# Kernel tuning notes

Measured on AMD Instinct MI355X. Metric: run time of the kernel, lower is better.

## Reference

```python
import jax, jax.numpy as jnp
import numpy as np
from jax import lax

B, C, K, H, W = 32, 256, 64, 64, 64  # batch, num_channels, num_corr_channels, spatial
IN = C + K  # enc input channels = 320
EPS = 1e-5


def setup_inputs() -> dict:
    key = jax.random.key(0)
    ks = jax.random.split(key, 20)
    n = lambda k, s, sc=0.05: jax.random.normal(k, s, dtype=jnp.float32) * sc
    return {
        "z": jax.random.normal(ks[0], (B, C, K), dtype=jnp.float32),
        "x": jax.random.normal(ks[1], (B, C, H, W), dtype=jnp.float32),
        "d": jax.random.normal(ks[2], (B, C, H, W), dtype=jnp.float32),
        # ConvBlock: depthwise [IN,1,3,3] + pointwise [C,IN]
        "dw_w": n(ks[3], (IN, 1, 3, 3), 0.1),
        "dw_b": n(ks[4], (IN,)),
        "pw_w": n(ks[5], (C, IN), 0.05),
        "pw_b": n(ks[6], (C,)),
        # BatchNorm2d (inference-mode running stats)
        "bn_gamma": 1.0 + n(ks[7], (C,)),
        "bn_beta": n(ks[8], (C,)),
        "bn_mean": n(ks[9], (C,)),
        "bn_var": 0.5 + jax.random.uniform(ks[10], (C,), dtype=jnp.float32),
        # SelfAttention: 1x1 conv projections + q/k/v linears
        "inp_w": n(ks[11], (C, C)), "inp_b": n(ks[12], (C,)),
        "q_w": n(ks[13], (C, C)), "q_b": n(ks[14], (C,)),
        "k_w": n(ks[15], (C, C)), "k_b": n(ks[16], (C,)),
        "v_w": n(ks[17], (C, C)), "v_b": n(ks[18], (C,)),
        "op_w": n(ks[19], (C, C)), "op_b": jnp.zeros((C,), jnp.float32),
    }


def reference(z, x, d, dw_w, dw_b, pw_w, pw_b, bn_gamma, bn_beta, bn_mean, bn_var,
              inp_w, inp_b, q_w, q_b, k_w, k_b, v_w, v_b, op_w, op_b):
    b, c, h, w = x.shape
    # correlation: z^T @ x_flat -> [b, K, h*w] -> [b, K, h, w]
    s = jnp.einsum('bck,bcn->bkn', z, x.reshape(b, c, h * w)).reshape(b, -1, h, w)
    s = jnp.concatenate([s, d], axis=1)  # [b, C+K, h, w]
    # depthwise 3x3 (pad 1) + pointwise 1x1
    s = lax.conv_general_dilated(s, dw_w, (1, 1), [(1, 1), (1, 1)],
                                 dimension_numbers=('NCHW', 'OIHW', 'NCHW'),
                                 feature_group_count=s.shape[1]) + dw_b[:, None, None]
    s = jnp.einsum('bihw,oi->bohw', s, pw_w) + pw_b[:, None, None]
    # BN (inference) + ReLU
    s = (s - bn_mean[:, None, None]) * lax.rsqrt(bn_var[:, None, None] + EPS)
    s = jnp.maximum(s * bn_gamma[:, None, None] + bn_beta[:, None, None], 0.0)
    # channel self-attention
    px = jnp.einsum('bchw,oc->bohw', s, inp_w) + inp_b[:, None, None]
    flat = px.reshape(b, c, h * w).transpose(0, 2, 1)  # [b, n, c]
    q = flat @ q_w.T + q_b
    k = flat @ k_w.T + k_b
    v = flat @ v_w.T + v_b
    score = jnp.einsum('bnc,bnd->bcd', q, k) / (c ** 0.5)  # [b, c, c]
    att = jax.nn.softmax(score, axis=2)
    weighted = jnp.einsum('bnc,bcd->bnd', v, att)  # values @ attention
    wt = weighted.transpose(0, 2, 1).reshape(b, c, h, w)
    out = jnp.einsum('bchw,oc->bohw', wt, op_w) + op_b[:, None, None]
    return out + s
```

## Files before the change

kernel.cpp:

```cpp
#include <hip/hip_runtime.h>

static constexpr int B_ = 32, C_ = 256, K_ = 64, H_ = 64, W_ = 64;
static constexpr int N_ = H_ * W_;
static constexpr int IN_ = C_ + K_;

__device__ __forceinline__ short f2bs(float f) {
  unsigned u = __builtin_bit_cast(unsigned, f);
  u += 0x7fffu + ((u >> 16) & 1u);
  return (short)(u >> 16);
}
__device__ __forceinline__ float bs2f(short s) {
  unsigned u = ((unsigned)(unsigned short)s) << 16;
  return __builtin_bit_cast(float, u);
}

typedef __attribute__((ext_vector_type(8))) short s8v;
typedef __attribute__((ext_vector_type(4))) short s4v;
typedef __attribute__((ext_vector_type(4))) float f4v;

static constexpr long long OB_XT   = 0;
static constexpr long long OB_ZT   = 67108864LL;
static constexpr long long OB_DWS  = 0;
static constexpr long long OB_DT   = 83886080LL;
static constexpr long long OB_PX   = 83886080LL;
static constexpr long long OB_CORR = 150994944LL;
static constexpr long long OB_G    = 150994944LL;
static constexpr long long OB_GB2  = 159383552LL;
static constexpr long long OB_S    = 167772160LL;
static constexpr long long OB_PXT  = 234881024LL;
static constexpr long long OB_ATT  = 301989888LL;
static constexpr long long OB_M2   = OB_ATT + 8388608LL;
static constexpr long long OB_M3   = OB_M2 + 8388608LL;
static constexpr long long OB_MISC = OB_M3 + 8388608LL;
static constexpr long long OB_PWW  = OB_MISC;
static constexpr long long OB_INPW = OB_PWW + 262144LL;
static constexpr long long OB_M3B  = OB_INPW + 262144LL;
static constexpr long long OB_R    = OB_M3B + 4194304LL;
static constexpr long long OB_U    = OB_R + 32768LL;
static constexpr long long OB_W2   = OB_U + 32768LL;
static constexpr long long OB_M2B  = OB_W2 + 32768LL;
static constexpr long long OB_B3   = OB_M2B + 32768LL;
static constexpr long long OB_BNS  = OB_B3 + 32768LL;
static constexpr long long OB_BNH  = OB_BNS + 2048LL;
static constexpr long long OB_QW2  = OB_BNH + 2048LL;
static constexpr long long OB_KWB  = OB_QW2 + 262144LL;
static constexpr long long OB_VWB  = OB_KWB + 131072LL;
static constexpr long long OB_OPWB = OB_VWB + 131072LL;
static constexpr long long OB_T1B  = OB_OPWB + 131072LL;
static constexpr long long OB_ATTT = OB_T1B + 4194304LL;
static constexpr long long OB_M2T  = OB_ATTT + 4194304LL;
static constexpr long long OB_VWT  = OB_M2T + 4194304LL;

__device__ __forceinline__ void gload16(const void* g, void* l) {
  __builtin_amdgcn_global_load_lds((const __attribute__((address_space(1))) void*)g,
                                   (__attribute__((address_space(3))) void*)l, 16, 0, 0);
}

template <int BN, int SPLIT, int EPI>
__global__ __launch_bounds__(256) void mgemm(
    const short* __restrict__ A, int lda, long long sA,
    const short* __restrict__ Bt, int ldb, long long sB,
    void* __restrict__ Cv, int ldc, long long sC,
    int Kd,
    const float* __restrict__ biasc, const float* __restrict__ shf,
    const float* __restrict__ biasr,
    const short* __restrict__ resT, int ldrt, long long sRT,
    short* __restrict__ outT, int ldt, long long sT)
{
  constexpr int JT = BN / 32;
  __shared__ short As[128 * 32];
  __shared__ short Bs[BN * 32];

  const int t = threadIdx.x;
  const int wv = t >> 6;
  const int lane = t & 63, quad = lane >> 4, lr = lane & 15;
  const int wm = wv >> 1, wn = wv & 1;
  const int m_off = wm * 64, n_off = wn * (BN / 2);

  const int n0 = blockIdx.x * BN;
  const int m0 = blockIdx.y * 128;
  const int bz = (SPLIT == 1) ? blockIdx.z : (blockIdx.z / SPLIT);
  const int sp = (SPLIT == 1) ? 0 : (blockIdx.z % SPLIT);
  const int koff = sp * Kd;

  A += (long long)bz * sA;
  Bt += (long long)bz * sB;

  const int arow = t >> 2;
  const int acol = (t & 3) << 3;

  f4v acc[4][JT];
#pragma unroll
  for (int i = 0; i < 4; ++i)
#pragma unroll
    for (int j = 0; j < JT; ++j) acc[i][j] = (f4v)0.f;

  for (int k0 = 0; k0 < Kd; k0 += 32) {
#pragma unroll
    for (int rr = 0; rr < 2; ++rr) {
      const short* gp = A + (long long)(m0 + rr * 64 + arow) * lda + koff + k0 + acol;
      gload16(gp, (char*)As + rr * 4096 + wv * 1024);
    }
#pragma unroll
    for (int rr = 0; rr < BN / 64; ++rr) {
      const short* gp = Bt + (long long)(n0 + rr * 64 + arow) * ldb + koff + k0 + acol;
      gload16(gp, (char*)Bs + rr * 4096 + wv * 1024);
    }
    __syncthreads();

    s8v af[4], bfv[JT];
#pragma unroll
    for (int i = 0; i < 4; ++i)
      af[i] = *(const s8v*)&As[(m_off + i * 16 + lr) * 32 + quad * 8];
#pragma unroll
    for (int j = 0; j < JT; ++j)
      bfv[j] = *(const s8v*)&Bs[(n_off + j * 16 + lr) * 32 + quad * 8];
#pragma unroll
    for (int i = 0; i < 4; ++i)
#pragma unroll
      for (int j = 0; j < JT; ++j)
        acc[i][j] = __builtin_amdgcn_mfma_f32_16x16x32_bf16(af[i], bfv[j], acc[i][j], 0, 0, 0);
    __syncthreads();
  }

  float* Cf = (float*)Cv;
  short* Cb = (short*)Cv;
  if (EPI & 1) Cb += (long long)bz * sC; else Cf += (long long)bz * sC;
  if (EPI & 16) resT += (long long)bz * sRT;
  if (EPI & 32) outT += (long long)bz * sT;

#pragma unroll
  for (int i = 0; i < 4; ++i) {
    const int mb = m0 + m_off + i * 16 + quad * 4;
#pragma unroll
    for (int j = 0; j < JT; ++j) {
      const int n = n0 + n_off + j * 16 + lr;
      float vr[4];
#pragma unroll
      for (int r = 0; r < 4; ++r) {
        float v = acc[i][j][r];
        if (EPI & 2) v += biasc[n];
        if (EPI & 4) v = fmaxf(fmaf(v, biasc[n], shf[n]), 0.f);
        if (EPI & 8) v += biasr[bz * 256 + mb + r];
        vr[r] = v;
      }
      if (EPI & 16) {
        s4v rv = *(const s4v*)(resT + (long long)n * ldrt + mb);
#pragma unroll
        for (int r = 0; r < 4; ++r) vr[r] += bs2f(rv[r]);
      }
      if (EPI & 32) {
        s4v tv;
#pragma unroll
        for (int r = 0; r < 4; ++r) tv[r] = f2bs(vr[r]);
        *(s4v*)(outT + (long long)n * ldt + mb) = tv;
      }
#pragma unroll
      for (int r = 0; r < 4; ++r) {
        if (EPI & 64) atomicAdd(&Cf[(long long)(mb + r) * ldc + n], vr[r]);
        else if (EPI & 1) Cb[(long long)(mb + r) * ldc + n] = f2bs(vr[r]);
        else Cf[(long long)(mb + r) * ldc + n] = vr[r];
      }
    }
  }
}

__global__ __launch_bounds__(256) void tcast(const float* __restrict__ in,
                                             short* __restrict__ out,
                                             int R, int Cc, long long sIn, long long sOut)
{
  __shared__ float tile[32][33];
  const int b = blockIdx.z;
  const int r0 = blockIdx.y * 32, c0 = blockIdx.x * 32;
  in += (long long)b * sIn;
  out += (long long)b * sOut;
  const int tx = threadIdx.x & 31, ty = threadIdx.x >> 5;
#pragma unroll
  for (int i = 0; i < 32; i += 8)
    tile[ty + i][tx] = in[(long long)(r0 + ty + i) * Cc + c0 + tx];
  __syncthreads();
#pragma unroll
  for (int i = 0; i < 32; i += 8)
    out[(long long)(c0 + ty + i) * R + r0 + tx] = f2bs(tile[tx][ty + i]);
}

__global__ void castw(const float* __restrict__ in, short* __restrict__ out, long long n)
{
  long long i = (long long)blockIdx.x * 256 + threadIdx.x;
  if (i < n) out[i] = f2bs(in[i]);
}

__global__ void castw2(const float* __restrict__ a, const float* __restrict__ b,
                       short* __restrict__ oa, short* __restrict__ ob)
{
  const int i = blockIdx.x * 256 + threadIdx.x;
  const int sel = i >> 16, off = i & 65535;
  const float* src = sel == 0 ? a : b;
  short* dst = sel == 0 ? oa : ob;
  dst[off] = f2bs(src[off]);
}

__global__ void qdup(const float* __restrict__ q, short* __restrict__ o)
{
  const int i = blockIdx.x * 256 + threadIdx.x;
  const short v = f2bs(q[i]);
  const int c = i >> 8, e = i & 255;
  o[c * 512 + e] = v;
  o[c * 512 + 256 + e] = v;
}

__global__ void ghilo(const float* __restrict__ G, short* __restrict__ g2)
{
  const long long i = (long long)blockIdx.x * 256 + threadIdx.x;
  const float g = G[i];
  const short h = f2bs(g);
  const short l = f2bs(g - bs2f(h));
  const long long row = i >> 8;
  const int e = (int)(i & 255);
  g2[row * 512 + e] = h;
  g2[row * 512 + 256 + e] = l;
}

__global__ __launch_bounds__(256) void dwconv4(const short* __restrict__ corr,
                                               const short* __restrict__ dt,
                                               const float* __restrict__ wgt,
                                               const float* __restrict__ bias,
                                               short* __restrict__ outp)
{
  __shared__ __align__(16) float wl[9 * IN_];
  __shared__ __align__(16) float bl[IN_];
  const int tid = threadIdx.x;
  for (int i = tid; i < 9 * IN_; i += 256) {
    const int ch = i / 9, tap = i % 9;
    wl[tap * IN_ + ch] = wgt[i];
  }
  for (int i = tid; i < IN_; i += 256) bl[i] = bias[i];
  __syncthreads();

  const int g = blockIdx.x * 256 + tid;
  const int b = blockIdx.y;
  const int cg = g % 40;
  const int rest = g / 40;
  const int x = rest & 63;
  const int y0 = (rest >> 6) << 2;
  const int ch0 = cg * 8;

  const short* base;
  int ldch, c0;
  if (cg < 8) { base = corr + (long long)b * N_ * K_; ldch = K_; c0 = ch0; }
  else        { base = dt   + (long long)b * N_ * C_; ldch = C_; c0 = ch0 - K_; }

  float acc[4][8];
  {
    float4 bv0 = *(const float4*)&bl[ch0];
    float4 bv1 = *(const float4*)&bl[ch0 + 4];
#pragma unroll
    for (int p = 0; p < 4; ++p) {
      acc[p][0] = bv0.x; acc[p][1] = bv0.y; acc[p][2] = bv0.z; acc[p][3] = bv0.w;
      acc[p][4] = bv1.x; acc[p][5] = bv1.y; acc[p][6] = bv1.z; acc[p][7] = bv1.w;
    }
  }

#pragma unroll
  for (int dx = -1; dx <= 1; ++dx) {
    const int xx = x + dx;
    if (xx < 0 || xx >= W_) continue;

    float wv[3][8];
#pragma unroll
    for (int dy1 = 0; dy1 < 3; ++dy1) {
      float4 wa = *(const float4*)&wl[(dy1 * 3 + (dx + 1)) * IN_ + ch0];
      float4 wb = *(const float4*)&wl[(dy1 * 3 + (dx + 1)) * IN_ + ch0 + 4];
      wv[dy1][0] = wa.x; wv[dy1][1] = wa.y; wv[dy1][2] = wa.z; wv[dy1][3] = wa.w;
      wv[dy1][4] = wb.x; wv[dy1][5] = wb.y; wv[dy1][6] = wb.z; wv[dy1][7] = wb.w;
    }

    s8v v[6];
#pragma unroll
    for (int ri = 0; ri < 6; ++ri) {
      const int yy = y0 - 1 + ri;
      if (yy >= 0 && yy < H_)
        v[ri] = *(const s8v*)(base + (long long)(yy * W_ + xx) * ldch + c0);
      else
        v[ri] = (s8v)0;
    }

#pragma unroll
    for (int ri = 0; ri < 6; ++ri) {
      float f[8];
#pragma unroll
      for (int j = 0; j < 8; ++j) f[j] = bs2f(v[ri][j]);
#pragma unroll
      for (int dy1 = 0; dy1 < 3; ++dy1) {
        const int p = ri - dy1;
        if (p < 0 || p > 3) continue;
#pragma unroll
        for (int j = 0; j < 8; ++j)
          acc[p][j] = fmaf(wv[dy1][j], f[j], acc[p][j]);
      }
    }
  }

#pragma unroll
  for (int p = 0; p < 4; ++p) {
    s8v o;
#pragma unroll
    for (int j = 0; j < 8; ++j) o[j] = f2bs(acc[p][j]);
    *(s8v*)(outp + ((long long)b * N_ + (y0 + p) * W_ + x) * IN_ + ch0) = o;
  }
}

__global__ void colsum(const short* __restrict__ px, float* __restrict__ r)
{
  const int b = blockIdx.y, c = threadIdx.x, chunk = blockIdx.x;
  const short* p = px + (long long)b * N_ * C_ + (long long)chunk * 512 * C_;
  float s = 0.f;
  for (int n = 0; n < 512; ++n) s += bs2f(p[(long long)n * C_ + c]);
  atomicAdd(&r[b * C_ + c], s);
}

__global__ void bncoef(const float* __restrict__ pwb, const float* __restrict__ g,
                       const float* __restrict__ bt, const float* __restrict__ mn,
                       const float* __restrict__ vr, float* __restrict__ scl,
                       float* __restrict__ shf)
{
  const int c = threadIdx.x;
  const float inv = rsqrtf(vr[c] + 1e-5f);
  const float sc = g[c] * inv;
  scl[c] = sc;
  shf[c] = (pwb[c] - mn[c]) * sc + bt[c];
}

__global__ void uwker(const float* __restrict__ qw, const float* __restrict__ kw,
                      const float* __restrict__ r, float* __restrict__ u,
                      float* __restrict__ w)
{
  const int b = blockIdx.x, c = threadIdx.x;
  __shared__ float rl[256];
  rl[c] = r[b * C_ + c];
  __syncthreads();
  float su = 0.f, sw = 0.f;
  for (int f = 0; f < C_; ++f) {
    const float rv = rl[f];
    su = fmaf(qw[c * C_ + f], rv, su);
    sw = fmaf(kw[c * C_ + f], rv, sw);
  }
  u[b * C_ + c] = su;
  w[b * C_ + c] = sw;
}

__global__ void fixsoftmax(float* __restrict__ att, const float* __restrict__ u,
                           const float* __restrict__ w, const float* __restrict__ qb,
                           const float* __restrict__ kb)
{
  const int c = blockIdx.x, b = blockIdx.y, d = threadIdx.x;
  const long long base = ((long long)b * C_ + c) * (long long)C_;
  const float qbc = qb[c];
  float val = 0.0625f * (att[base + d] + u[b * C_ + c] * kb[d] + qbc * w[b * C_ + d] +
                         (float)N_ * qbc * kb[d]);
  __shared__ float red[256];
  red[d] = val;
  __syncthreads();
  for (int k = 128; k > 0; k >>= 1) {
    if (d < k) red[d] = fmaxf(red[d], red[d + k]);
    __syncthreads();
  }
  const float mx = red[0];
  __syncthreads();
  const float e = expf(val - mx);
  red[d] = e;
  __syncthreads();
  for (int k = 128; k > 0; k >>= 1) {
    if (d < k) red[d] += red[d + k];
    __syncthreads();
  }
  att[base + d] = e / red[0];
}

__global__ void m2bker(const float* __restrict__ att, const float* __restrict__ vb,
                       float* __restrict__ m2b)
{
  const int b = blockIdx.x, d = threadIdx.x;
  const float* a = att + (long long)b * C_ * C_;
  float s = 0.f;
  for (int c = 0; c < C_; ++c) s = fmaf(a[c * C_ + d], vb[c], s);
  m2b[b * C_ + d] = s;
}

__global__ void b3ker(const float* __restrict__ opw, const float* __restrict__ m2b,
                      const float* __restrict__ opb, float* __restrict__ b3)
{
  const int b = blockIdx.x, o = threadIdx.x;
  __shared__ float m[256];
  m[o] = m2b[b * C_ + o];
  __syncthreads();
  float s = opb[o];
  for (int d = 0; d < C_; ++d) s = fmaf(opw[o * C_ + d], m[d], s);
  b3[b * C_ + o] = s;
}

extern "C" void kernel_launch(void* const* d_in, const int* in_sizes, int n_in,
                              void* d_out, int out_size, void* d_ws, size_t ws_size,
                              hipStream_t stream)
{
  (void)in_sizes; (void)n_in; (void)out_size; (void)ws_size;
  const float* z     = (const float*)d_in[0];
  const float* x     = (const float*)d_in[1];
  const float* dimg  = (const float*)d_in[2];
  const float* dw_w  = (const float*)d_in[3];
  const float* dw_b  = (const float*)d_in[4];
  const float* pw_w  = (const float*)d_in[5];
  const float* pw_b  = (const float*)d_in[6];
  const float* bn_g  = (const float*)d_in[7];
  const float* bn_b  = (const float*)d_in[8];
  const float* bn_m  = (const float*)d_in[9];
  const float* bn_v  = (const float*)d_in[10];
  const float* inp_w = (const float*)d_in[11];
  const float* inp_b = (const float*)d_in[12];
  const float* q_w   = (const float*)d_in[13];
  const float* q_b   = (const float*)d_in[14];
  const float* k_w   = (const float*)d_in[15];
  const float* k_b   = (const float*)d_in[16];
  const float* v_w   = (const float*)d_in[17];
  const float* v_b   = (const float*)d_in[18];
  const float* op_w  = (const float*)d_in[19];
  const float* op_b  = (const float*)d_in[20];
  float* out = (float*)d_out;

  char* ws = (char*)d_ws;
  short* xt    = (short*)(ws + OB_XT);
  short* zt    = (short*)(ws + OB_ZT);
  short* dws   = (short*)(ws + OB_DWS);
  short* dt    = (short*)(ws + OB_DT);
  short* px_b  = (short*)(ws + OB_PX);
  short* corr  = (short*)(ws + OB_CORR);
  float* G     = (float*)(ws + OB_G);
  short* Gb2   = (short*)(ws + OB_GB2);
  short* s_b   = (short*)(ws + OB_S);
  short* pxT   = (short*)(ws + OB_PXT);
  float* att   = (float*)(ws + OB_ATT);
  short* M2scr = (short*)(ws + OB_M2);
  short* pw_wb = (short*)(ws + OB_PWW);
  short* inp_wb= (short*)(ws + OB_INPW);
  short* M3b   = (short*)(ws + OB_M3B);
  float* r     = (float*)(ws + OB_R);
  float* u     = (float*)(ws + OB_U);
  float* w2    = (float*)(ws + OB_W2);
  float* m2b   = (float*)(ws + OB_M2B);
  float* b3    = (float*)(ws + OB_B3);
  float* bns   = (float*)(ws + OB_BNS);
  float* bnh   = (float*)(ws + OB_BNH);
  short* q_wb2 = (short*)(ws + OB_QW2);
  short* k_wb  = (short*)(ws + OB_KWB);
  short* op_wb = (short*)(ws + OB_OPWB);
  short* T1b   = (short*)(ws + OB_T1B);
  short* attT  = (short*)(ws + OB_ATTT);
  short* M2T   = (short*)(ws + OB_M2T);
  short* v_wT  = (short*)(ws + OB_VWT);

  const long long sNC = (long long)N_ * C_;
  const long long sNK = (long long)N_ * K_;
  const long long sNI = (long long)N_ * IN_;
  const long long sCC = (long long)C_ * C_;

  bncoef<<<1, 256, 0, stream>>>(pw_b, bn_g, bn_b, bn_m, bn_v, bns, bnh);
  castw<<<(IN_ * C_ + 255) / 256, 256, 0, stream>>>(pw_w, pw_wb, IN_ * C_);
  castw<<<(C_ * C_ + 255) / 256, 256, 0, stream>>>(inp_w, inp_wb, C_ * C_);
  qdup<<<256, 256, 0, stream>>>(q_w, q_wb2);
  castw2<<<512, 256, 0, stream>>>(k_w, op_w, k_wb, op_wb);
  tcast<<<dim3(8, 8, 1), 256, 0, stream>>>(v_w, v_wT, C_, C_, 0, 0);
  tcast<<<dim3(N_ / 32, C_ / 32, B_), 256, 0, stream>>>(x, xt, C_, N_, sNC, sNC);
  tcast<<<dim3(K_ / 32, C_ / 32, B_), 256, 0, stream>>>(z, zt, C_, K_, (long long)C_ * K_,
                                                        (long long)C_ * K_);
  tcast<<<dim3(N_ / 32, C_ / 32, B_), 256, 0, stream>>>(dimg, dt, C_, N_, sNC, sNC);

  mgemm<64, 1, 1><<<dim3(1, 32, B_), 256, 0, stream>>>(
      xt, C_, sNC, zt, C_, (long long)K_ * C_, corr, K_, sNK, C_,
      nullptr, nullptr, nullptr, nullptr, 0, 0, nullptr, 0, 0);

  dwconv4<<<dim3(160, B_), 256, 0, stream>>>(corr, dt, dw_w, dw_b, dws);

  mgemm<128, 1, (1 | 4)><<<dim3(2, 32, B_), 256, 0, stream>>>(
      dws, IN_, sNI, pw_wb, IN_, 0, s_b, C_, sNC, IN_,
      bns, bnh, nullptr, nullptr, 0, 0, nullptr, 0, 0);

  mgemm<128, 1, (1 | 2 | 32)><<<dim3(2, 32, B_), 256, 0, stream>>>(
      s_b, C_, sNC, inp_wb, C_, 0, px_b, C_, sNC, C_,
      inp_b, nullptr, nullptr, nullptr, 0, 0, pxT, N_, sNC);

  hipMemsetAsync(r, 0, B_ * C_ * sizeof(float), stream);
  colsum<<<dim3(8, B_), 256, 0, stream>>>(px_b, r);

  hipMemsetAsync(G, 0, (size_t)B_ * C_ * C_ * sizeof(float), stream);
  mgemm<128, 8, 64><<<dim3(2, 2, B_ * 8), 256, 0, stream>>>(
      pxT, N_, sNC, pxT, N_, sNC, G, C_, sCC, N_ / 8,
      nullptr, nullptr, nullptr, nullptr, 0, 0, nullptr, 0, 0);

  ghilo<<<8192, 256, 0, stream>>>(G, Gb2);

  uwker<<<B_, 256, 0, stream>>>(q_w, k_w, r, u, w2);

  mgemm<128, 1, 1><<<dim3(2, 2, B_), 256, 0, stream>>>(
      q_wb2, 512, 0, Gb2, 512, 256LL * 512, T1b, C_, sCC, 512,
      nullptr, nullptr, nullptr, nullptr, 0, 0, nullptr, 0, 0);

  mgemm<128, 1, 0><<<dim3(2, 2, B_), 256, 0, stream>>>(
      T1b, C_, sCC, k_wb, C_, 0, att, C_, sCC, C_,
      nullptr, nullptr, nullptr, nullptr, 0, 0, nullptr, 0, 0);

  fixsoftmax<<<dim3(C_, B_), 256, 0, stream>>>(att, u, w2, q_b, k_b);

  tcast<<<dim3(8, 8, B_), 256, 0, stream>>>(att, attT, C_, C_, sCC, sCC);

  mgemm<128, 1, (1 | 32)><<<dim3(2, 2, B_), 256, 0, stream>>>(
      attT, C_, sCC, v_wT, C_, 0, M2scr, C_, sCC, C_,
      nullptr, nullptr, nullptr, nullptr, 0, 0, M2T, C_, sCC);

  mgemm<128, 1, 1><<<dim3(2, 2, B_), 256, 0, stream>>>(
      op_wb, C_, 0, M2T, C_, sCC, M3b, C_, sCC, C_,
      nullptr, nullptr, nullptr, nullptr, 0, 0, nullptr, 0, 0);

  m2bker<<<B_, 256, 0, stream>>>(att, v_b, m2b);
  b3ker<<<B_, 256, 0, stream>>>(op_w, m2b, op_b, b3);

  mgemm<128, 1, (8 | 16)><<<dim3(32, 2, B_), 256, 0, stream>>>(
      M3b, C_, sCC, px_b, C_, sNC, out, N_, sNC, C_,
      nullptr, nullptr, b3, s_b, C_, sNC, nullptr, 0, 0);
}
```

Before: 853.3 us.

## Vectorize transpose-cast, merge weight prep kernels, remap dwconv thread layout

Replaces the 32x32 scalar transpose-cast kernel with a 64x64 tile that uses float4 loads and 8-wide bf16 stores, cutting the number of memory instructions for the large x and d transposes. Folds the BN coefficient kernel and the four weight-cast kernels into one launch to cut launch overhead. Remaps dwconv threads so each wavefront covers 8 channel groups by 8 x positions, aiming for more contiguous global reads. The wider transpose tile uses more shared memory per block, which may lower occupancy.

```diff
diff --git a/kernel.cpp b/kernel.cpp
--- a/kernel.cpp
+++ b/kernel.cpp
@@ -165,48 +165,72 @@
   }
 }
 
-__global__ __launch_bounds__(256) void tcast(const float* __restrict__ in,
-                                             short* __restrict__ out,
-                                             int R, int Cc, long long sIn, long long sOut)
-{
-  __shared__ float tile[32][33];
+__global__ __launch_bounds__(256) void tcast8(const float* __restrict__ in,
+                                              short* __restrict__ out,
+                                              int R, int Cc, long long sIn, long long sOut)
+{
+  __shared__ __align__(16) float tile[64][68];
   const int b = blockIdx.z;
-  const int r0 = blockIdx.y * 32, c0 = blockIdx.x * 32;
+  const int c0 = blockIdx.x * 64, r0 = blockIdx.y * 64;
   in += (long long)b * sIn;
   out += (long long)b * sOut;
-  const int tx = threadIdx.x & 31, ty = threadIdx.x >> 5;
-#pragma unroll
-  for (int i = 0; i < 32; i += 8)
-    tile[ty + i][tx] = in[(long long)(r0 + ty + i) * Cc + c0 + tx];
-  __syncthreads();
-#pragma unroll
-  for (int i = 0; i < 32; i += 8)
-    out[(long long)(c0 + ty + i) * R + r0 + tx] = f2bs(tile[tx][ty + i]);
-}
-
-__global__ void castw(const float* __restrict__ in, short* __restrict__ out, long long n)
-{
-  long long i = (long long)blockIdx.x * 256 + threadIdx.x;
-  if (i < n) out[i] = f2bs(in[i]);
-}
-
-__global__ void castw2(const float* __restrict__ a, const float* __restrict__ b,
-                       short* __restrict__ oa, short* __restrict__ ob)
-{
-  const int i = blockIdx.x * 256 + threadIdx.x;
-  const int sel = i >> 16, off = i & 65535;
-  const float* src = sel == 0 ? a : b;
-  short* dst = sel == 0 ? oa : ob;
-  dst[off] = f2bs(src[off]);
-}
-
-__global__ void qdup(const float* __restrict__ q, short* __restrict__ o)
-{
-  const int i = blockIdx.x * 256 + threadIdx.x;
-  const short v = f2bs(q[i]);
-  const int c = i >> 8, e = i & 255;
-  o[c * 512 + e] = v;
-  o[c * 512 + 256 + e] = v;
+  const int t = threadIdx.x;
+
+  const int lr = t >> 2;
+  const int lcb = (t & 3) << 2;
+#pragma unroll
+  for (int i = 0; i < 4; ++i) {
+    const int col = lcb + i * 16;
+    *(float4*)&tile[lr][col] = *(const float4*)(in + (long long)(r0 + lr) * Cc + c0 + col);
+  }
+  __syncthreads();
+
+  const int cc = t >> 2;
+  const int rq = (t & 3) << 3;
+#pragma unroll
+  for (int i = 0; i < 2; ++i) {
+    const int rr = rq + i * 32;
+    s8v o;
+#pragma unroll
+    for (int j = 0; j < 8; ++j) o[j] = f2bs(tile[rr + j][cc]);
+    *(s8v*)(out + (long long)(c0 + cc) * R + r0 + rr) = o;
+  }
+}
+
+__global__ void prepw(const float* __restrict__ pwb, const float* __restrict__ bng,
+                      const float* __restrict__ bnb, const float* __restrict__ bnm,
+                      const float* __restrict__ bnv, float* __restrict__ bns,
+                      float* __restrict__ bnh,
+                      const float* __restrict__ pw_w, short* __restrict__ pw_wb,
+                      const float* __restrict__ inp_w, short* __restrict__ inp_wb,
+                      const float* __restrict__ q_w, short* __restrict__ q_wb2,
+                      const float* __restrict__ k_w, short* __restrict__ k_wb,
+                      const float* __restrict__ op_w, short* __restrict__ op_wb)
+{
+  const int bx = blockIdx.x, t = threadIdx.x;
+  if (bx == 0) {
+    const float inv = rsqrtf(bnv[t] + 1e-5f);
+    const float sc = bng[t] * inv;
+    bns[t] = sc;
+    bnh[t] = (pwb[t] - bnm[t]) * sc + bnb[t];
+    return;
+  }
+  int i = (bx - 1) * 256 + t;
+  if (i < 81920) { pw_wb[i] = f2bs(pw_w[i]); return; }
+  i -= 81920;
+  if (i < 65536) { inp_wb[i] = f2bs(inp_w[i]); return; }
+  i -= 65536;
+  if (i < 65536) {
+    const short v = f2bs(q_w[i]);
+    const int c = i >> 8, e = i & 255;
+    q_wb2[c * 512 + e] = v;
+    q_wb2[c * 512 + 256 + e] = v;
+    return;
+  }
+  i -= 65536;
+  if (i < 65536) { k_wb[i] = f2bs(k_w[i]); return; }
+  i -= 65536;
+  op_wb[i] = f2bs(op_w[i]);
 }
 
 __global__ void ghilo(const float* __restrict__ G, short* __restrict__ g2)
@@ -221,7 +245,7 @@
   g2[row * 512 + 256 + e] = l;
 }
 
-__global__ __launch_bounds__(256) void dwconv4(const short* __restrict__ corr,
+__global__ __launch_bounds__(256) void dwconv5(const short* __restrict__ corr,
                                                const short* __restrict__ dt,
                                                const float* __restrict__ wgt,
                                                const float* __restrict__ bias,
@@ -237,18 +261,25 @@
   for (int i = tid; i < IN_; i += 256) bl[i] = bias[i];
   __syncthreads();
 
-  const int g = blockIdx.x * 256 + tid;
+  const int lane = tid & 63;
+  const int wv = tid >> 6;
+  const int cgsub = lane & 7;
+  const int xsub = lane >> 3;
+
+  const int wid = blockIdx.x * 4 + wv;
   const int b = blockIdx.y;
-  const int cg = g % 40;
-  const int rest = g / 40;
-  const int x = rest & 63;
-  const int y0 = (rest >> 6) << 2;
+  const int cgo = wid % 5;
+  const int rest = wid / 5;
+  const int x = ((rest & 7) << 3) + xsub;
+  const int y0 = (rest >> 3) << 2;
+
+  const int cg = cgo * 8 + cgsub;
   const int ch0 = cg * 8;
 
   const short* base;
   int ldch, c0;
-  if (cg < 8) { base = corr + (long long)b * N_ * K_; ldch = K_; c0 = ch0; }
-  else        { base = dt   + (long long)b * N_ * C_; ldch = C_; c0 = ch0 - K_; }
+  if (cgo == 0) { base = corr + (long long)b * N_ * K_; ldch = K_; c0 = ch0; }
+  else          { base = dt   + (long long)b * N_ * C_; ldch = C_; c0 = ch0 - K_; }
 
   float acc[4][8];
   {
@@ -266,13 +297,13 @@
     const int xx = x + dx;
     if (xx < 0 || xx >= W_) continue;
 
-    float wv[3][8];
+    float wv3[3][8];
 #pragma unroll
     for (int dy1 = 0; dy1 < 3; ++dy1) {
       float4 wa = *(const float4*)&wl[(dy1 * 3 + (dx + 1)) * IN_ + ch0];
       float4 wb = *(const float4*)&wl[(dy1 * 3 + (dx + 1)) * IN_ + ch0 + 4];
-      wv[dy1][0] = wa.x; wv[dy1][1] = wa.y; wv[dy1][2] = wa.z; wv[dy1][3] = wa.w;
-      wv[dy1][4] = wb.x; wv[dy1][5] = wb.y; wv[dy1][6] = wb.z; wv[dy1][7] = wb.w;
+      wv3[dy1][0] = wa.x; wv3[dy1][1] = wa.y; wv3[dy1][2] = wa.z; wv3[dy1][3] = wa.w;
+      wv3[dy1][4] = wb.x; wv3[dy1][5] = wb.y; wv3[dy1][6] = wb.z; wv3[dy1][7] = wb.w;
     }
 
     s8v v[6];
@@ -296,7 +327,7 @@
         if (p < 0 || p > 3) continue;
 #pragma unroll
         for (int j = 0; j < 8; ++j)
-          acc[p][j] = fmaf(wv[dy1][j], f[j], acc[p][j]);
+          acc[p][j] = fmaf(wv3[dy1][j], f[j], acc[p][j]);
       }
     }
   }
@@ -317,18 +348,6 @@
   float s = 0.f;
   for (int n = 0; n < 512; ++n) s += bs2f(p[(long long)n * C_ + c]);
   atomicAdd(&r[b * C_ + c], s);
-}
-
-__global__ void bncoef(const float* __restrict__ pwb, const float* __restrict__ g,
-                       const float* __restrict__ bt, const float* __restrict__ mn,
-                       const float* __restrict__ vr, float* __restrict__ scl,
-                       float* __restrict__ shf)
-{
-  const int c = threadIdx.x;
-  const float inv = rsqrtf(vr[c] + 1e-5f);
-  const float sc = g[c] * inv;
-  scl[c] = sc;
-  shf[c] = (pwb[c] - mn[c]) * sc + bt[c];
 }
 
 __global__ void uwker(const float* __restrict__ qw, const float* __restrict__ kw,
@@ -463,22 +482,20 @@
   const long long sNI = (long long)N_ * IN_;
   const long long sCC = (long long)C_ * C_;
 
-  bncoef<<<1, 256, 0, stream>>>(pw_b, bn_g, bn_b, bn_m, bn_v, bns, bnh);
-  castw<<<(IN_ * C_ + 255) / 256, 256, 0, stream>>>(pw_w, pw_wb, IN_ * C_);
-  castw<<<(C_ * C_ + 255) / 256, 256, 0, stream>>>(inp_w, inp_wb, C_ * C_);
-  qdup<<<256, 256, 0, stream>>>(q_w, q_wb2);
-  castw2<<<512, 256, 0, stream>>>(k_w, op_w, k_wb, op_wb);
-  tcast<<<dim3(8, 8, 1), 256, 0, stream>>>(v_w, v_wT, C_, C_, 0, 0);
-  tcast<<<dim3(N_ / 32, C_ / 32, B_), 256, 0, stream>>>(x, xt, C_, N_, sNC, sNC);
-  tcast<<<dim3(K_ / 32, C_ / 32, B_), 256, 0, stream>>>(z, zt, C_, K_, (long long)C_ * K_,
-                                                        (long long)C_ * K_);
-  tcast<<<dim3(N_ / 32, C_ / 32, B_), 256, 0, stream>>>(dimg, dt, C_, N_, sNC, sNC);
+  prepw<<<1345, 256, 0, stream>>>(pw_b, bn_g, bn_b, bn_m, bn_v, bns, bnh,
+                                  pw_w, pw_wb, inp_w, inp_wb, q_w, q_wb2,
+                                  k_w, k_wb, op_w, op_wb);
+  tcast8<<<dim3(4, 4, 1), 256, 0, stream>>>(v_w, v_wT, C_, C_, 0, 0);
+  tcast8<<<dim3(N_ / 64, C_ / 64, B_), 256, 0, stream>>>(x, xt, C_, N_, sNC, sNC);
+  tcast8<<<dim3(1, C_ / 64, B_), 256, 0, stream>>>(z, zt, C_, K_, (long long)C_ * K_,
+                                                   (long long)C_ * K_);
+  tcast8<<<dim3(N_ / 64, C_ / 64, B_), 256, 0, stream>>>(dimg, dt, C_, N_, sNC, sNC);
 
   mgemm<64, 1, 1><<<dim3(1, 32, B_), 256, 0, stream>>>(
       xt, C_, sNC, zt, C_, (long long)K_ * C_, corr, K_, sNK, C_,
       nullptr, nullptr, nullptr, nullptr, 0, 0, nullptr, 0, 0);
 
-  dwconv4<<<dim3(160, B_), 256, 0, stream>>>(corr, dt, dw_w, dw_b, dws);
+  dwconv5<<<dim3(160, B_), 256, 0, stream>>>(corr, dt, dw_w, dw_b, dws);
 
   mgemm<128, 1, (1 | 4)><<<dim3(2, 32, B_), 256, 0, stream>>>(
       dws, IN_, sNI, pw_wb, IN_, 0, s_b, C_, sNC, IN_,
@@ -510,7 +527,7 @@
 
   fixsoftmax<<<dim3(C_, B_), 256, 0, stream>>>(att, u, w2, q_b, k_b);
 
-  tcast<<<dim3(8, 8, B_), 256, 0, stream>>>(att, attT, C_, C_, sCC, sCC);
+  tcast8<<<dim3(4, 4, B_), 256, 0, stream>>>(att, attT, C_, C_, sCC, sCC);
 
   mgemm<128, 1, (1 | 32)><<<dim3(2, 2, B_), 256, 0, stream>>>(
       attT, C_, sCC, v_wT, C_, 0, M2scr, C_, sCC, C_,
```

Result: faster. 835.0 us (-2.1%).
